# Kernel tuning notes

Measured on AMD Instinct MI355X. Metric: run time of the kernel, lower is better.

## Reference

```python
import jax, jax.numpy as jnp
import numpy as np

VOCAB, E, H = 32000, 512, 512
B, T = 256, 128
EPS = 1e-12  # F.normalize eps


def setup_inputs() -> dict:
    key = jax.random.key(0)
    ks = jax.random.split(key, 9)
    s_e = 1.0 / np.sqrt(E)
    s_h = 1.0 / np.sqrt(H)
    captions = jax.random.randint(ks[0], (B, T), 0, VOCAB, dtype=jnp.int32)
    emb = jax.random.normal(ks[1], (VOCAB, E), dtype=jnp.float32)
    # fused input->gates weight [E,4H] (gate order: i, f, o, g) and bias [4H]
    Wx = jax.random.uniform(ks[2], (E, 4 * H), jnp.float32, -s_e, s_e)
    bx = jax.random.uniform(ks[3], (4 * H,), jnp.float32, -s_e, s_e)
    # fused hidden->gates weight [H,4H] and bias [4H]
    Uh = jax.random.uniform(ks[4], (H, 4 * H), jnp.float32, -s_h, s_h)
    bu = jax.random.uniform(ks[5], (4 * H,), jnp.float32, -s_h, s_h)
    fcW = jax.random.uniform(ks[6], (H, E), jnp.float32, -s_h, s_h)
    fcb = jax.random.uniform(ks[7], (E,), jnp.float32, -s_h, s_h)
    return {"captions": captions, "emb": emb, "Wx": Wx, "bx": bx,
            "Uh": Uh, "bu": bu, "fcW": fcW, "fcb": fcb}


def reference(captions, emb, Wx, bx, Uh, bu, fcW, fcb):
    # padding_idx=0: embedding row 0 is zero
    emb = emb.at[0].set(0.0)
    x = emb[captions]  # [B,T,E]
    # precompute all input-to-gate projections in one fused GEMM
    xg = jnp.einsum('bte,ef->btf', x, Wx) + bx  # [B,T,4H]

    def step(carry, xg_t):
        h, c = carry
        g = xg_t + h @ Uh + bu  # [B,4H]
        i, f, o, gg = jnp.split(g, 4, axis=-1)
        c = jax.nn.sigmoid(f) * c + jax.nn.sigmoid(i) * jnp.tanh(gg)
        h = jax.nn.sigmoid(o) * jnp.tanh(c)
        return (h, c), None

    h0 = jnp.zeros((captions.shape[0], H), xg.dtype)
    (h, _), _ = jax.lax.scan(step, (h0, h0), jnp.swapaxes(xg, 0, 1))
    out = h @ fcW + fcb  # [B,E]
    norm = jnp.sqrt(jnp.sum(out * out, axis=1, keepdims=True))
    return out / jnp.maximum(norm, EPS)
```

## Files before the change

### kernel.cpp

```cpp
#include <hip/hip_runtime.h>

#define B_ 256
#define T_ 128
#define E_ 512
#define H_ 512
#define NG 2048
#define NB 256
#define NT 512

typedef __attribute__((ext_vector_type(8))) short bf16x8;
typedef __attribute__((ext_vector_type(4))) float f32x4;

__device__ __forceinline__ short f2bf(float f) {
  union { float f; unsigned u; } x; x.f = f;
  unsigned r = x.u + 0x7FFFu + ((x.u >> 16) & 1u);
  return (short)(r >> 16);
}
__device__ __forceinline__ float bf2f(short s) {
  union { unsigned u; float f; } x;
  x.u = ((unsigned)(unsigned short)s) << 16; return x.f;
}
__device__ __forceinline__ float sigm(float x) { return 1.0f / (1.0f + __expf(-x)); }

__global__ __launch_bounds__(256) void prep_w(const float* __restrict__ Wx,
                                              const float* __restrict__ Uh,
                                              short* __restrict__ Wt) {
  __shared__ float tile[64][65];
  const int k0 = blockIdx.x * 64;
  const int j0 = blockIdx.y * 64;
  const int tx = threadIdx.x & 63, ty = threadIdx.x >> 6;
#pragma unroll
  for (int r = 0; r < 16; ++r) {
    int k = k0 + r * 4 + ty;
    float v = (k < 512) ? Wx[(size_t)k * NG + j0 + tx]
                        : Uh[(size_t)(k - 512) * NG + j0 + tx];
    tile[r * 4 + ty][tx] = v;
  }
  __syncthreads();
#pragma unroll
  for (int r = 0; r < 16; ++r) {
    int j = j0 + r * 4 + ty;
    Wt[(size_t)j * 1024 + k0 + tx] = f2bf(tile[tx][r * 4 + ty]);
  }
}

__global__ __launch_bounds__(256) void stage_x(const int* __restrict__ captions,
                                               const float* __restrict__ emb,
                                               short* __restrict__ xs) {
  const int bid = blockIdx.x;
  const int t = bid >> 8, b = bid & 255;
  const int tok = captions[b * T_ + t];
  short* o = xs + (size_t)bid * E_;
  const float* src = emb + (size_t)tok * E_;
  int e0 = threadIdx.x, e1 = threadIdx.x + 256;
  if (tok) { o[e0] = f2bf(src[e0]); o[e1] = f2bf(src[e1]); }
  else     { o[e0] = 0;             o[e1] = 0; }
}

__global__ __launch_bounds__(NT, 1) void lstm_all(
    const short* __restrict__ xs,
    const short* __restrict__ Wt,
    const float* __restrict__ bx, const float* __restrict__ bu,
    unsigned* __restrict__ h0, unsigned* __restrict__ h1, unsigned* __restrict__ h2,
    unsigned* __restrict__ flags) {
  __shared__ short wlds[4 * 16 * 1024];
  __shared__ float red[2][2][4][16][16];
  __shared__ float gbuf[2][4][16][16];

  const int tid = threadIdx.x;
  const int wid = tid >> 6, lane = tid & 63;
  const int l15 = lane & 15, l4 = lane >> 4;
  const int mh = wid & 1, kq = wid >> 1;
  const int mg = blockIdx.x & 7, jt = blockIdx.x >> 3;
  const int j0 = jt * 16;
  const int rA = mg * 32 + mh * 16 + l15;

  for (int r8 = 0; r8 < 8; ++r8) {
    const int row = wid * 8 + r8;
    const int g = row >> 4, col = row & 15;
    const short* src = Wt + (size_t)(g * 512 + j0 + col) * 1024;
#pragma unroll
    for (int rep = 0; rep < 2; ++rep) {
      int soff = lane * 8 + rep * 512;
      *(bf16x8*)&wlds[row * 1024 + (soff ^ ((col & 7) << 3))] =
          *(const bf16x8*)(src + soff);
    }
  }

  const int mh2 = tid >> 8, rr = (tid >> 4) & 15, jj = tid & 15;
  const int J = j0 + jj;
  const float bi  = bx[J] + bu[J];
  const float bf_ = bx[512 + J] + bu[512 + J];
  const float bo  = bx[1024 + J] + bu[1024 + J];
  const float bg  = bx[1536 + J] + bu[1536 + J];
  const int Rrow = mg * 32 + mh2 * 16 + rr;
  const int hpk = Rrow * 256 + ((j0 + jj) >> 1);
  float c_reg = 0.f;

  unsigned* hb[3] = {h0, h1, h2};
  unsigned* fl = flags + mg * 32 * 32;

  __syncthreads();

  for (int t = 0; t < T_; ++t) {
    const unsigned* hin = hb[t % 3];
    unsigned* hout = hb[(t + 1) % 3];

    bf16x8 af[8];
    if (kq < 2) {
      const short* ab = xs + ((size_t)t * B_ + rA) * E_ + kq * 256 + l4 * 8;
#pragma unroll
      for (int ks = 0; ks < 8; ++ks) af[ks] = *(const bf16x8*)(ab + ks * 32);
    } else {
      if (lane < 32) {
        while (__hip_atomic_load(&fl[lane * 32], __ATOMIC_RELAXED,
                                 __HIP_MEMORY_SCOPE_AGENT) < (unsigned)t)
          __builtin_amdgcn_s_sleep(1);
      }
      asm volatile("" ::: "memory");
      const unsigned long long* ab = (const unsigned long long*)
          (hin + (size_t)rA * 256 + (kq - 2) * 128 + l4 * 4);
#pragma unroll
      for (int ks = 0; ks < 8; ++ks) {
        union { bf16x8 v; unsigned long long u[2]; } tmp;
        tmp.u[0] = __hip_atomic_load(ab + ks * 8,     __ATOMIC_RELAXED, __HIP_MEMORY_SCOPE_AGENT);
        tmp.u[1] = __hip_atomic_load(ab + ks * 8 + 1, __ATOMIC_RELAXED, __HIP_MEMORY_SCOPE_AGENT);
        af[ks] = tmp.v;
      }
    }

    f32x4 acc[4] = {{0,0,0,0},{0,0,0,0},{0,0,0,0},{0,0,0,0}};
#pragma unroll
    for (int ks = 0; ks < 8; ++ks) {
      const int swz = (kq * 256 + ks * 32 + l4 * 8) ^ ((l15 & 7) << 3);
#pragma unroll
      for (int g = 0; g < 4; ++g) {
        bf16x8 bw = *(const bf16x8*)&wlds[(g * 16 + l15) * 1024 + swz];
        acc[g] = __builtin_amdgcn_mfma_f32_16x16x32_bf16(af[ks], bw, acc[g], 0, 0, 0);
      }
    }

    if (kq & 1) {
      const int slot = kq >> 1;
#pragma unroll
      for (int g = 0; g < 4; ++g)
#pragma unroll
        for (int r = 0; r < 4; ++r)
          red[mh][slot][g][l4 * 4 + r][l15] = acc[g][r];
    }
    __syncthreads();
    if (kq == 0) {
#pragma unroll
      for (int g = 0; g < 4; ++g)
#pragma unroll
        for (int r = 0; r < 4; ++r)
          acc[g][r] += red[mh][0][g][l4 * 4 + r][l15];
    } else if (kq == 2) {
#pragma unroll
      for (int g = 0; g < 4; ++g)
#pragma unroll
        for (int r = 0; r < 4; ++r)
          red[mh][1][g][l4 * 4 + r][l15] += acc[g][r];
    }
    __syncthreads();
    if (kq == 0) {
#pragma unroll
      for (int g = 0; g < 4; ++g)
#pragma unroll
        for (int r = 0; r < 4; ++r)
          gbuf[mh][g][l4 * 4 + r][l15] = acc[g][r] + red[mh][1][g][l4 * 4 + r][l15];
    }
    __syncthreads();

    {
      float iv = gbuf[mh2][0][rr][jj] + bi;
      float fv = gbuf[mh2][1][rr][jj] + bf_;
      float ov = gbuf[mh2][2][rr][jj] + bo;
      float gv = gbuf[mh2][3][rr][jj] + bg;
      float cn = sigm(fv) * c_reg + sigm(iv) * tanhf(gv);
      c_reg = cn;
      unsigned mine = (unsigned)(unsigned short)f2bf(sigm(ov) * tanhf(cn));
      unsigned other = (unsigned)__shfl_xor((int)mine, 1, 64);
      if (!(jj & 1))
        __hip_atomic_store(&hout[hpk], mine | (other << 16),
                           __ATOMIC_RELAXED, __HIP_MEMORY_SCOPE_AGENT);
    }

    asm volatile("s_waitcnt vmcnt(0)" ::: "memory");
    __syncthreads();
    if (t < T_ - 1 && tid == 0)
      __hip_atomic_store(&fl[jt * 32], (unsigned)(t + 1),
                         __ATOMIC_RELAXED, __HIP_MEMORY_SCOPE_AGENT);
  }
}

__global__ __launch_bounds__(256) void final_fc(const short* __restrict__ h,
                                                const float* __restrict__ fcW,
                                                const float* __restrict__ fcb,
                                                float* __restrict__ out) {
  const int b = blockIdx.x, tid = threadIdx.x;
  __shared__ float hrow[512];
  __shared__ float red[256];
  for (int k = tid; k < 512; k += 256) hrow[k] = bf2f(h[b * 512 + k]);
  __syncthreads();
  float a0 = fcb[tid], a1 = fcb[tid + 256];
  for (int k = 0; k < 512; ++k) {
    float hv = hrow[k];
    a0 += hv * fcW[(size_t)k * 512 + tid];
    a1 += hv * fcW[(size_t)k * 512 + tid + 256];
  }
  red[tid] = a0 * a0 + a1 * a1;
  __syncthreads();
  for (int s = 128; s > 0; s >>= 1) {
    if (tid < s) red[tid] += red[tid + s];
    __syncthreads();
  }
  float scale = 1.0f / fmaxf(sqrtf(red[0]), 1e-12f);
  out[(size_t)b * 512 + tid] = a0 * scale;
  out[(size_t)b * 512 + tid + 256] = a1 * scale;
}

extern "C" void kernel_launch(void* const* d_in, const int* in_sizes, int n_in,
                              void* d_out, int out_size, void* d_ws, size_t ws_size,
                              hipStream_t stream) {
  const int*   captions = (const int*)d_in[0];
  const float* emb      = (const float*)d_in[1];
  const float* Wx       = (const float*)d_in[2];
  const float* bx       = (const float*)d_in[3];
  const float* Uh       = (const float*)d_in[4];
  const float* bu       = (const float*)d_in[5];
  const float* fcW      = (const float*)d_in[6];
  const float* fcb      = (const float*)d_in[7];
  float* out = (float*)d_out;

  char* ws = (char*)d_ws;
  size_t off = 0;
  auto alloc = [&](size_t bytes) {
    char* p = ws + off;
    off += (bytes + 255) & ~(size_t)255;
    return p;
  };
  short*    Wt    = (short*)alloc((size_t)NG * 1024 * 2);
  short*    xs    = (short*)alloc((size_t)T_ * B_ * E_ * 2);
  unsigned* h0    = (unsigned*)alloc((size_t)B_ * H_ * 2);
  unsigned* h1    = (unsigned*)alloc((size_t)B_ * H_ * 2);
  unsigned* h2    = (unsigned*)alloc((size_t)B_ * H_ * 2);
  unsigned* flags = (unsigned*)alloc(8 * 32 * 32 * 4);

  hipMemsetAsync(h0, 0, (size_t)B_ * H_ * 2, stream);
  hipMemsetAsync(flags, 0, 8 * 32 * 32 * 4, stream);

  prep_w<<<dim3(16, 32), 256, 0, stream>>>(Wx, Uh, Wt);
  stage_x<<<T_ * B_, 256, 0, stream>>>(captions, emb, xs);

  void* kargs[] = {(void*)&xs, (void*)&Wt, (void*)&bx, (void*)&bu,
                   (void*)&h0, (void*)&h1, (void*)&h2, (void*)&flags};
  hipLaunchCooperativeKernel((const void*)lstm_all, dim3(NB), dim3(NT),
                             kargs, 0, stream);

  final_fc<<<B_, 256, 0, stream>>>((const short*)h2, fcW, fcb, out);
}
```

Baseline: 802.9 us.

## Tag hidden-state words with step epoch and keep gate weights in registers

Measured after the change: 1.101 ms. +37.1%, slower.

```diff
diff --git a/kernel.cpp b/kernel.cpp
--- a/kernel.cpp
+++ b/kernel.cpp
@@ -10,6 +10,7 @@
 
 typedef __attribute__((ext_vector_type(8))) short bf16x8;
 typedef __attribute__((ext_vector_type(4))) float f32x4;
+typedef unsigned long long u64;
 
 __device__ __forceinline__ short f2bf(float f) {
   union { float f; unsigned u; } x; x.f = f;
@@ -21,6 +22,11 @@
   x.u = ((unsigned)(unsigned short)s) << 16; return x.f;
 }
 __device__ __forceinline__ float sigm(float x) { return 1.0f / (1.0f + __expf(-x)); }
+__device__ __forceinline__ float tanh_(float x) {
+  float cx = fminf(fmaxf(x, -9.f), 9.f);
+  float e = __expf(2.f * cx);
+  return (e - 1.f) / (e + 1.f);
+}
 
 __global__ __launch_bounds__(256) void prep_w(const float* __restrict__ Wx,
                                               const float* __restrict__ Uh,
@@ -57,15 +63,13 @@
   else     { o[e0] = 0;             o[e1] = 0; }
 }
 
-__global__ __launch_bounds__(NT, 1) void lstm_all(
+__global__ __launch_bounds__(NT, 2) void lstm_all(
     const short* __restrict__ xs,
     const short* __restrict__ Wt,
     const float* __restrict__ bx, const float* __restrict__ bu,
-    unsigned* __restrict__ h0, unsigned* __restrict__ h1, unsigned* __restrict__ h2,
-    unsigned* __restrict__ flags) {
-  __shared__ short wlds[4 * 16 * 1024];
-  __shared__ float red[2][2][4][16][16];
-  __shared__ float gbuf[2][4][16][16];
+    u64* __restrict__ hb0, u64* __restrict__ hb1) {
+  __shared__ float red[2][3][4][16][17];
+  __shared__ float gbuf[2][4][16][17];
 
   const int tid = threadIdx.x;
   const int wid = tid >> 6, lane = tid & 63;
@@ -75,16 +79,13 @@
   const int j0 = jt * 16;
   const int rA = mg * 32 + mh * 16 + l15;
 
-  for (int r8 = 0; r8 < 8; ++r8) {
-    const int row = wid * 8 + r8;
-    const int g = row >> 4, col = row & 15;
-    const short* src = Wt + (size_t)(g * 512 + j0 + col) * 1024;
-#pragma unroll
-    for (int rep = 0; rep < 2; ++rep) {
-      int soff = lane * 8 + rep * 512;
-      *(bf16x8*)&wlds[row * 1024 + (soff ^ ((col & 7) << 3))] =
-          *(const bf16x8*)(src + soff);
-    }
+  bf16x8 bfr[4][8];
+#pragma unroll
+  for (int g = 0; g < 4; ++g) {
+    const short* wp = Wt + (size_t)(g * 512 + j0 + l15) * 1024 + kq * 256 + l4 * 8;
+#pragma unroll
+    for (int ks = 0; ks < 8; ++ks)
+      bfr[g][ks] = *(const bf16x8*)(wp + ks * 32);
   }
 
   const int mh2 = tid >> 8, rr = (tid >> 4) & 15, jj = tid & 15;
@@ -94,59 +95,62 @@
   const float bo  = bx[1024 + J] + bu[1024 + J];
   const float bg  = bx[1536 + J] + bu[1536 + J];
   const int Rrow = mg * 32 + mh2 * 16 + rr;
-  const int hpk = Rrow * 256 + ((j0 + jj) >> 1);
+  const int hpk = Rrow * 256 + ((j0 + (jj & ~1)) >> 1);
   float c_reg = 0.f;
 
-  unsigned* hb[3] = {h0, h1, h2};
-  unsigned* fl = flags + mg * 32 * 32;
-
-  __syncthreads();
-
   for (int t = 0; t < T_; ++t) {
-    const unsigned* hin = hb[t % 3];
-    unsigned* hout = hb[(t + 1) % 3];
-
-    bf16x8 af[8];
+    u64* hout = (t & 1) ? hb1 : hb0;
+    const u64* hin = (t & 1) ? hb0 : hb1;
+
+    f32x4 acc[4] = {{0,0,0,0},{0,0,0,0},{0,0,0,0},{0,0,0,0}};
+
     if (kq < 2) {
       const short* ab = xs + ((size_t)t * B_ + rA) * E_ + kq * 256 + l4 * 8;
+      bf16x8 af[8];
 #pragma unroll
       for (int ks = 0; ks < 8; ++ks) af[ks] = *(const bf16x8*)(ab + ks * 32);
-    } else {
-      if (lane < 32) {
-        while (__hip_atomic_load(&fl[lane * 32], __ATOMIC_RELAXED,
-                                 __HIP_MEMORY_SCOPE_AGENT) < (unsigned)t)
-          __builtin_amdgcn_s_sleep(1);
+#pragma unroll
+      for (int ks = 0; ks < 8; ++ks)
+#pragma unroll
+        for (int g = 0; g < 4; ++g)
+          acc[g] = __builtin_amdgcn_mfma_f32_16x16x32_bf16(af[ks], bfr[g][ks], acc[g], 0, 0, 0);
+    } else if (t > 0) {
+      const u64* hp = hin + (size_t)rA * 256 + (kq - 2) * 128 + l4 * 4;
+      const unsigned exp_ = (unsigned)t;
+      u64 w[32];
+#pragma unroll
+      for (int ks = 0; ks < 8; ++ks)
+#pragma unroll
+        for (int i = 0; i < 4; ++i)
+          w[ks * 4 + i] = __hip_atomic_load(hp + ks * 16 + i,
+                                            __ATOMIC_RELAXED, __HIP_MEMORY_SCOPE_AGENT);
+#pragma unroll
+      for (int ks = 0; ks < 8; ++ks)
+#pragma unroll
+        for (int i = 0; i < 4; ++i) {
+          u64 v = w[ks * 4 + i];
+          while ((unsigned)(v >> 32) != exp_)
+            v = __hip_atomic_load(hp + ks * 16 + i,
+                                  __ATOMIC_RELAXED, __HIP_MEMORY_SCOPE_AGENT);
+          w[ks * 4 + i] = v;
+        }
+#pragma unroll
+      for (int ks = 0; ks < 8; ++ks) {
+        union { bf16x8 v; unsigned u[4]; } fa;
+#pragma unroll
+        for (int i = 0; i < 4; ++i) fa.u[i] = (unsigned)w[ks * 4 + i];
+#pragma unroll
+        for (int g = 0; g < 4; ++g)
+          acc[g] = __builtin_amdgcn_mfma_f32_16x16x32_bf16(fa.v, bfr[g][ks], acc[g], 0, 0, 0);
       }
-      asm volatile("" ::: "memory");
-      const unsigned long long* ab = (const unsigned long long*)
-          (hin + (size_t)rA * 256 + (kq - 2) * 128 + l4 * 4);
-#pragma unroll
-      for (int ks = 0; ks < 8; ++ks) {
-        union { bf16x8 v; unsigned long long u[2]; } tmp;
-        tmp.u[0] = __hip_atomic_load(ab + ks * 8,     __ATOMIC_RELAXED, __HIP_MEMORY_SCOPE_AGENT);
-        tmp.u[1] = __hip_atomic_load(ab + ks * 8 + 1, __ATOMIC_RELAXED, __HIP_MEMORY_SCOPE_AGENT);
-        af[ks] = tmp.v;
-      }
-    }
-
-    f32x4 acc[4] = {{0,0,0,0},{0,0,0,0},{0,0,0,0},{0,0,0,0}};
-#pragma unroll
-    for (int ks = 0; ks < 8; ++ks) {
-      const int swz = (kq * 256 + ks * 32 + l4 * 8) ^ ((l15 & 7) << 3);
-#pragma unroll
-      for (int g = 0; g < 4; ++g) {
-        bf16x8 bw = *(const bf16x8*)&wlds[(g * 16 + l15) * 1024 + swz];
-        acc[g] = __builtin_amdgcn_mfma_f32_16x16x32_bf16(af[ks], bw, acc[g], 0, 0, 0);
-      }
-    }
-
-    if (kq & 1) {
-      const int slot = kq >> 1;
+    }
+
+    if (kq) {
 #pragma unroll
       for (int g = 0; g < 4; ++g)
 #pragma unroll
         for (int r = 0; r < 4; ++r)
-          red[mh][slot][g][l4 * 4 + r][l15] = acc[g][r];
+          red[mh][kq - 1][g][l4 * 4 + r][l15] = acc[g][r];
     }
     __syncthreads();
     if (kq == 0) {
@@ -154,21 +158,10 @@
       for (int g = 0; g < 4; ++g)
 #pragma unroll
         for (int r = 0; r < 4; ++r)
-          acc[g][r] += red[mh][0][g][l4 * 4 + r][l15];
-    } else if (kq == 2) {
-#pragma unroll
-      for (int g = 0; g < 4; ++g)
-#pragma unroll
-        for (int r = 0; r < 4; ++r)
-          red[mh][1][g][l4 * 4 + r][l15] += acc[g][r];
-    }
-    __syncthreads();
-    if (kq == 0) {
-#pragma unroll
-      for (int g = 0; g < 4; ++g)
-#pragma unroll
-        for (int r = 0; r < 4; ++r)
-          gbuf[mh][g][l4 * 4 + r][l15] = acc[g][r] + red[mh][1][g][l4 * 4 + r][l15];
+          gbuf[mh][g][l4 * 4 + r][l15] = acc[g][r]
+              + red[mh][0][g][l4 * 4 + r][l15]
+              + red[mh][1][g][l4 * 4 + r][l15]
+              + red[mh][2][g][l4 * 4 + r][l15];
     }
     __syncthreads();
 
@@ -177,31 +170,30 @@
       float fv = gbuf[mh2][1][rr][jj] + bf_;
       float ov = gbuf[mh2][2][rr][jj] + bo;
       float gv = gbuf[mh2][3][rr][jj] + bg;
-      float cn = sigm(fv) * c_reg + sigm(iv) * tanhf(gv);
+      float cn = sigm(fv) * c_reg + sigm(iv) * tanh_(gv);
       c_reg = cn;
-      unsigned mine = (unsigned)(unsigned short)f2bf(sigm(ov) * tanhf(cn));
+      unsigned mine = (unsigned)(unsigned short)f2bf(sigm(ov) * tanh_(cn));
       unsigned other = (unsigned)__shfl_xor((int)mine, 1, 64);
-      if (!(jj & 1))
-        __hip_atomic_store(&hout[hpk], mine | (other << 16),
-                           __ATOMIC_RELAXED, __HIP_MEMORY_SCOPE_AGENT);
-    }
-
-    asm volatile("s_waitcnt vmcnt(0)" ::: "memory");
-    __syncthreads();
-    if (t < T_ - 1 && tid == 0)
-      __hip_atomic_store(&fl[jt * 32], (unsigned)(t + 1),
-                         __ATOMIC_RELAXED, __HIP_MEMORY_SCOPE_AGENT);
-  }
-}
-
-__global__ __launch_bounds__(256) void final_fc(const short* __restrict__ h,
+      if (!(jj & 1)) {
+        u64 val = (u64)(mine | (other << 16)) | (((u64)(unsigned)(t + 1)) << 32);
+        __hip_atomic_store(&hout[hpk], val, __ATOMIC_RELAXED, __HIP_MEMORY_SCOPE_AGENT);
+      }
+    }
+  }
+}
+
+__global__ __launch_bounds__(256) void final_fc(const u64* __restrict__ h,
                                                 const float* __restrict__ fcW,
                                                 const float* __restrict__ fcb,
                                                 float* __restrict__ out) {
   const int b = blockIdx.x, tid = threadIdx.x;
   __shared__ float hrow[512];
   __shared__ float red[256];
-  for (int k = tid; k < 512; k += 256) hrow[k] = bf2f(h[b * 512 + k]);
+  {
+    u64 w = h[(size_t)b * 256 + tid];
+    hrow[tid * 2]     = bf2f((short)(w & 0xFFFF));
+    hrow[tid * 2 + 1] = bf2f((short)((w >> 16) & 0xFFFF));
+  }
   __syncthreads();
   float a0 = fcb[tid], a1 = fcb[tid + 256];
   for (int k = 0; k < 512; ++k) {
@@ -240,23 +232,21 @@
     off += (bytes + 255) & ~(size_t)255;
     return p;
   };
-  short*    Wt    = (short*)alloc((size_t)NG * 1024 * 2);
-  short*    xs    = (short*)alloc((size_t)T_ * B_ * E_ * 2);
-  unsigned* h0    = (unsigned*)alloc((size_t)B_ * H_ * 2);
-  unsigned* h1    = (unsigned*)alloc((size_t)B_ * H_ * 2);
-  unsigned* h2    = (unsigned*)alloc((size_t)B_ * H_ * 2);
-  unsigned* flags = (unsigned*)alloc(8 * 32 * 32 * 4);
-
-  hipMemsetAsync(h0, 0, (size_t)B_ * H_ * 2, stream);
-  hipMemsetAsync(flags, 0, 8 * 32 * 32 * 4, stream);
+  short* Wt  = (short*)alloc((size_t)NG * 1024 * 2);
+  short* xs  = (short*)alloc((size_t)T_ * B_ * E_ * 2);
+  u64*   hb0 = (u64*)alloc((size_t)B_ * 256 * 8);
+  u64*   hb1 = (u64*)alloc((size_t)B_ * 256 * 8);
+
+  hipMemsetAsync(hb0, 0, (size_t)B_ * 256 * 8, stream);
+  hipMemsetAsync(hb1, 0, (size_t)B_ * 256 * 8, stream);
 
   prep_w<<<dim3(16, 32), 256, 0, stream>>>(Wx, Uh, Wt);
   stage_x<<<T_ * B_, 256, 0, stream>>>(captions, emb, xs);
 
   void* kargs[] = {(void*)&xs, (void*)&Wt, (void*)&bx, (void*)&bu,
-                   (void*)&h0, (void*)&h1, (void*)&h2, (void*)&flags};
+                   (void*)&hb0, (void*)&hb1};
   hipLaunchCooperativeKernel((const void*)lstm_all, dim3(NB), dim3(NT),
                              kargs, 0, stream);
 
-  final_fc<<<B_, 256, 0, stream>>>((const short*)h2, fcW, fcb, out);
-}
+  final_fc<<<B_, 256, 0, stream>>>(hb1, fcW, fcb, out);
+}
```
